# Kernel optimization log

Measured on AMD Instinct MI355X. Metric: run time of the kernel, lower is better.

Reference implementation:

```python
import jax, jax.numpy as jnp
import numpy as np

H_DIM = 256
N_HEADS = 8
HALF = H_DIM // 2

def _lin(x, W, b):
    # torch nn.Linear: y = x @ W.T + b
    y = x @ W.T
    return y + b if b is not None else y

def setup_inputs() -> dict:
    key = jax.random.key(0)
    ks = jax.random.split(key, 16)
    s = 0.02
    d = {
        'x': jax.random.normal(ks[0], (16, H_DIM, 32, 32), jnp.float32),
        'q1_w': jax.random.normal(ks[1], (HALF, HALF), jnp.float32) * s,
        'q1_b': jnp.zeros((HALF,), jnp.float32),
        'q2_w': jax.random.normal(ks[2], (HALF, HALF), jnp.float32) * s,
        'q2_b': jnp.zeros((HALF,), jnp.float32),
        'k1_w': jax.random.normal(ks[3], (HALF, HALF), jnp.float32) * s,
        'k1_b': jnp.zeros((HALF,), jnp.float32),
        'k2_w': jax.random.normal(ks[4], (HALF, HALF), jnp.float32) * s,
        'k2_b': jnp.zeros((HALF,), jnp.float32),
        'v1_w': jax.random.normal(ks[5], (HALF, HALF), jnp.float32) * s,
        'v1_b': jnp.zeros((HALF,), jnp.float32),
        'v2_w': jax.random.normal(ks[6], (HALF, HALF), jnp.float32) * s,
        'v2_b': jnp.zeros((HALF,), jnp.float32),
        'proj1_w': jax.random.normal(ks[7], (HALF, HALF), jnp.float32) * s,
        'proj1_b': jnp.zeros((HALF,), jnp.float32),
        'proj2_w': jax.random.normal(ks[8], (HALF, HALF), jnp.float32) * s,
        'proj2_b': jnp.zeros((HALF,), jnp.float32),
        'logit_scale': jnp.log(10.0 * jnp.ones((N_HEADS, 1, 1), jnp.float32)),
        'mlp_w1': jax.random.normal(ks[9], (128, 2), jnp.float32) * s,
        'mlp_b1': jnp.zeros((128,), jnp.float32),
        'mlp_w2': jax.random.normal(ks[10], (N_HEADS, 128), jnp.float32) * s,
    }
    return d

def _rel_pos_index(h, w):
    # static (numpy) relative position index, shape [N, N]
    ch, cw = np.meshgrid(np.arange(h), np.arange(w), indexing='ij')
    coords = np.stack([ch.reshape(-1), cw.reshape(-1)])  # [2, N]
    rel = coords[:, :, None] - coords[:, None, :]         # [2, N, N]
    rel = rel.transpose(1, 2, 0)
    rel[:, :, 0] += h - 1
    rel[:, :, 1] += w - 1
    return rel[:, :, 0] * (2 * w - 1) + rel[:, :, 1]

def _forward(x, q1_w, q1_b, q2_w, q2_b, k1_w, k1_b, k2_w, k2_b,
             v1_w, v1_b, v2_w, v2_b, proj1_w, proj1_b, proj2_w, proj2_b,
             logit_scale, mlp_w1, mlp_b1, mlp_w2):
    b, c, h, w = x.shape
    N = h * w
    nh = N_HEADS
    hd = c // nh
    x3 = jnp.transpose(x, (0, 2, 3, 1)).reshape(b, N, c)
    x0, x1 = x3[..., :c // 2], x3[..., c // 2:]

    def qkv(W0, b0, W1, b1):
        t = jnp.concatenate([x0 + _lin(x0, W0, b0), x1 + _lin(x1, W1, b1)], axis=-1)
        return t.reshape(b, N, nh, hd).transpose(0, 2, 1, 3)  # [b, nh, N, hd]

    q = qkv(q1_w, q1_b, q2_w, q2_b)
    k = qkv(k1_w, k1_b, k2_w, k2_b)
    v = qkv(v1_w, v1_b, v2_w, v2_b)

    eps = 1e-12
    qn = q / jnp.maximum(jnp.linalg.norm(q, axis=-1, keepdims=True), eps)
    kn = k / jnp.maximum(jnp.linalg.norm(k, axis=-1, keepdims=True), eps)
    attn = jnp.einsum('bhnd,bhmd->bhnm', qn, kn)  # cosine similarity
    scale = jnp.exp(jnp.minimum(logit_scale, jnp.log(1.0 / 0.01)))  # [nh,1,1]
    attn = attn * scale[None]

    # continuous relative-position bias (CPB) table via small MLP
    rch = jnp.arange(-(h - 1), h, dtype=jnp.float32) / (h - 1 + 1e-8)
    rcw = jnp.arange(-(w - 1), w, dtype=jnp.float32) / (w - 1 + 1e-8)
    gh, gw = jnp.meshgrid(rch, rcw, indexing='ij')
    tab = jnp.stack([gh, gw], axis=-1) * 3.2               # [2h-1, 2w-1, 2]
    tab = jnp.sign(tab) * (1.0 - jnp.exp(-jnp.abs(tab)))
    tab = jax.nn.relu(_lin(tab, mlp_w1, mlp_b1))
    tab = _lin(tab, mlp_w2, None).reshape(-1, nh)          # [(2h-1)(2w-1), nh]

    idx = jnp.asarray(_rel_pos_index(h, w))                # [N, N]
    bias = tab[idx.reshape(-1)].reshape(N, N, nh).transpose(2, 0, 1)
    bias = 16.0 * jax.nn.sigmoid(bias)
    attn = attn + bias[None]

    attn = jax.nn.softmax(attn, axis=-1)
    out = jnp.einsum('bhnm,bhmd->bhnd', attn, v).transpose(0, 2, 1, 3).reshape(b, N, c)
    o0, o1 = out[..., :c // 2], out[..., c // 2:]
    out = jnp.concatenate([_lin(o0, proj1_w, proj1_b), _lin(o1, proj2_w, proj2_b)], axis=-1)
    return out.reshape(b, h, w, c).transpose(0, 3, 1, 2)

def reference(x, q1_w, q1_b, q2_w, q2_b, k1_w, k1_b, k2_w, k2_b,
              v1_w, v1_b, v2_w, v2_b, proj1_w, proj1_b, proj2_w, proj2_b,
              logit_scale, mlp_w1, mlp_b1, mlp_w2):
    return _forward(x, q1_w, q1_b, q2_w, q2_b, k1_w, k1_b, k2_w, k2_b,
                    v1_w, v1_b, v2_w, v2_b, proj1_w, proj1_b, proj2_w, proj2_b,
                    logit_scale, mlp_w1, mlp_b1, mlp_w2)
```

## Files before the change

kernel.cpp:

```cpp
#include <hip/hip_runtime.h>
#include <cmath>


typedef _Float16 half_t;
typedef __attribute__((ext_vector_type(4))) _Float16 half4;
typedef __attribute__((ext_vector_type(8))) _Float16 half8;
typedef __attribute__((ext_vector_type(4))) float float4v;

static __device__ __forceinline__ float4v mfma16(half8 a, half8 b, float4v c) {
  return __builtin_amdgcn_mfma_f32_16x16x32_f16(a, b, c, 0, 0, 0);
}

struct PtrArr8 { const float* p[8]; };

__global__ __launch_bounds__(256) void prep_w(PtrArr8 wsrc, PtrArr8 bsrc,
                                              half_t* __restrict__ wf,
                                              float* __restrict__ bws) {
  int y = blockIdx.y;
  const float* src = nullptr;
  const float* bs = nullptr;
#pragma unroll
  for (int i = 0; i < 8; i++)
    if (i == y) { src = wsrc.p[i]; bs = bsrc.p[i]; }
  int flat = (blockIdx.x * 256 + threadIdx.x) * 4;
  float4 w = *(const float4*)(src + flat);
  int j = flat >> 7, k = flat & 127;
  if (y < 6) {
    if (k == j)     w.x += 1.0f;
    if (k + 1 == j) w.y += 1.0f;
    if (k + 2 == j) w.z += 1.0f;
    if (k + 3 == j) w.w += 1.0f;
  }
  half4 h;
  h[0] = (half_t)w.x;
  h[1] = (half_t)w.y;
  h[2] = (half_t)w.z;
  h[3] = (half_t)w.w;
  int ng = j >> 4, l = j & 15, ks = k >> 5, quad = (k >> 3) & 3, o8 = k & 7;
  *(half4*)(wf + y * 16384 + ((ng * 4 + ks) * 64 + quad * 16 + l) * 8 + o8) =
      h;
  if (blockIdx.x == 0 && threadIdx.x < 128)
    bws[y * 128 + threadIdx.x] = bs[threadIdx.x];
}

__global__ __launch_bounds__(256) void bias_mlp(const float* __restrict__ w1,
                                                const float* __restrict__ b1,
                                                const float* __restrict__ w2,
                                                const float* __restrict__ ls,
                                                float* __restrict__ tabh2) {
  __shared__ float sw1[256];
  __shared__ float sb1[128];
  __shared__ float sw2[1024];
  int t = threadIdx.x;
  sw1[t] = w1[t];
  if (t < 128) sb1[t] = b1[t];
  for (int i = t; i < 1024; i += 256) sw2[i] = w2[i];
  __syncthreads();
  int p = blockIdx.x * 256 + t;
  if (p >= 3969) return;
  int ph = p / 63, pw = p % 63;
  float t0 = (float)(ph - 31) * (3.2f / 31.0f);
  float t1 = (float)(pw - 31) * (3.2f / 31.0f);
  t0 = copysignf(1.0f - __expf(-fabsf(t0)), t0);
  t1 = copysignf(1.0f - __expf(-fabsf(t1)), t1);
  float acc[8];
#pragma unroll
  for (int hh = 0; hh < 8; hh++) acc[hh] = 0.0f;
  for (int j = 0; j < 128; j++) {
    float hj = fmaxf(0.0f, t0 * sw1[2 * j] + t1 * sw1[2 * j + 1] + sb1[j]);
#pragma unroll
    for (int hh = 0; hh < 8; hh++) acc[hh] += hj * sw2[hh * 128 + j];
  }
  const float L2E = 1.44269504f;
#pragma unroll
  for (int hh = 0; hh < 8; hh++) {
    float scale = __expf(fminf(ls[hh], 4.6051702f));
    float c14 = 14.0f - (scale + 16.0f) * L2E;
    float bias = 16.0f / (1.0f + __expf(-acc[hh]));
    tabh2[hh * 3969 + p] = bias * L2E + c14;
  }
}

__global__ __launch_bounds__(256, 4) void qkv_mfma(
    const float* __restrict__ x, const half_t* __restrict__ wfrag,
    const float* __restrict__ lscale, const float* __restrict__ bws,
    half_t* __restrict__ qf, half_t* __restrict__ kf,
    half_t* __restrict__ vf) {
  __shared__ half_t tbuf[4608];
  int t = threadIdx.x;
  int lane = t & 63, wv = t >> 6, l = lane & 15, quad = lane >> 4;
  int rw = wv & 1, cw = wv >> 1;
  int hf = blockIdx.y;
  int m0 = blockIdx.x * 32;
  int b = m0 >> 10, n0 = m0 & 1023;

  half8 afr[4];
  {
    const float* xb =
        x + ((size_t)b * 256 + hf * 128) * 1024 + n0 + rw * 16 + l;
#pragma unroll
    for (int ks = 0; ks < 4; ks++) {
      half8 a;
#pragma unroll
      for (int j = 0; j < 8; j++)
        a[j] = (half_t)xb[(size_t)(ks * 32 + quad * 8 + j) * 1024];
      afr[ks] = a;
    }
  }

  for (int op = 0; op < 3; op++) {
    int combo = op * 2 + hf;
    const half_t* wfb = wfrag + combo * 16384;
    float4v acc[4];
#pragma unroll
    for (int ngl = 0; ngl < 4; ngl++) {
      int ng = cw * 4 + ngl;
      float4v c = {0.f, 0.f, 0.f, 0.f};
#pragma unroll
      for (int ks = 0; ks < 4; ks++) {
        half8 bfrag =
            *(const half8*)(wfb + ((ng * 4 + ks) * 64 + lane) * 8);
        c = mfma16(afr[ks], bfrag, c);
      }
      acc[ngl] = c;
    }
#pragma unroll
    for (int ngl = 0; ngl < 4; ngl++) {
      float bb = bws[combo * 128 + (cw * 4 + ngl) * 16 + l];
#pragma unroll
      for (int r2 = 0; r2 < 4; r2++) acc[ngl][r2] += bb;
    }
    if (op < 2) {
#pragma unroll
      for (int hgl = 0; hgl < 2; hgl++) {
        float sc = 1.0f;
        if (op == 0)
          sc = __expf(fminf(lscale[hf * 4 + cw * 2 + hgl], 4.6051702f)) *
               1.44269504f;
#pragma unroll
        for (int r2 = 0; r2 < 4; r2++) {
          float ss = acc[2 * hgl][r2] * acc[2 * hgl][r2] +
                     acc[2 * hgl + 1][r2] * acc[2 * hgl + 1][r2];
          ss += __shfl_xor(ss, 1, 64);
          ss += __shfl_xor(ss, 2, 64);
          ss += __shfl_xor(ss, 4, 64);
          ss += __shfl_xor(ss, 8, 64);
          float rn = sc / fmaxf(sqrtf(ss), 1e-12f);
          acc[2 * hgl][r2] *= rn;
          acc[2 * hgl + 1][r2] *= rn;
        }
      }
#pragma unroll
      for (int ngl = 0; ngl < 4; ngl++)
#pragma unroll
        for (int r2 = 0; r2 < 4; r2++)
          tbuf[(rw * 16 + quad * 4 + r2) * 136 + (cw * 4 + ngl) * 16 + l] =
              (half_t)acc[ngl][r2];
      __syncthreads();
      half_t* dst = (op == 0) ? qf : kf;
#pragma unroll
      for (int i = 0; i < 2; i++) {
        int idx = t + 256 * i;
        int row = idx >> 4, colc = (idx & 15) * 8;
        half8 vv = *(const half8*)(tbuf + row * 136 + colc);
        int head = hf * 4 + (colc >> 5), d = colc & 31;
        *(half8*)(dst + (((size_t)b * 8 + head) * 1024 + n0 + row) * 32 + d) =
            vv;
      }
      __syncthreads();
    } else {
#pragma unroll
      for (int ngl = 0; ngl < 4; ngl++) {
        int col = (cw * 4 + ngl) * 16 + l;
        half4 hv;
#pragma unroll
        for (int r2 = 0; r2 < 4; r2++) hv[r2] = (half_t)acc[ngl][r2];
        *(half4*)(tbuf + col * 36 + rw * 16 + quad * 4) = hv;
      }
      __syncthreads();
#pragma unroll
      for (int i = 0; i < 8; i++) {
        int idx = t + 256 * i;
        int col = idx >> 4, rp = idx & 15;
        unsigned int val = *(const unsigned int*)(tbuf + col * 36 + rp * 2);
        int head = hf * 4 + (col >> 5);
        int d = col & 31;
        *(unsigned int*)((char*)vf +
                         (((((size_t)b * 8 + head) * 32 + d) * 1024) + n0 +
                          rp * 2) * 2) = val;
      }
    }
  }
}

__global__ __launch_bounds__(256) void attn_mfma(
    const half_t* __restrict__ qf, const half_t* __restrict__ kf,
    const half_t* __restrict__ vf, const float* __restrict__ tabh2,
    half_t* __restrict__ ao) {
  __shared__ float sb2[35 * 63];
  __shared__ half_t pa[4 * 16 * 80];

  int id = blockIdx.x;
  int qo = id >> 7;
  int bh = id & 127;
  int h = bh & 7, b = bh >> 3;
  int t = threadIdx.x;
  int lane = t & 63, wv = t >> 6, l = lane & 15, quad = lane >> 4;
  size_t bhs = (size_t)b * 8 + h;
  const half_t* kbase = kf + bhs * 1024 * 32;
  const half_t* vbase = vf + bhs * 32 * 1024;

  for (int i = t; i < 2205; i += 256)
    sb2[i] = tabh2[h * 3969 + qo * 252 + i];

  int row0 = qo * 128 + wv * 32;
  half8 qfr[2];
#pragma unroll
  for (int s = 0; s < 2; s++)
    qfr[s] = *(const half8*)(qf + (bhs * 1024 + row0 + s * 16 + l) * 32 +
                             quad * 8);

  float4v o0[2], o1[2];
  float run_l[2];
#pragma unroll
  for (int s = 0; s < 2; s++) {
    o0[s] = (float4v){0.f, 0.f, 0.f, 0.f};
    o1[s] = (float4v){0.f, 0.f, 0.f, 0.f};
    run_l[s] = 0.0f;
  }
  half_t* paw = pa + wv * 16 * 80;
  __syncthreads();

#pragma unroll 2
  for (int kt = 0; kt < 16; kt++) {
    half8 kfr[4], v0fr[2], v1fr[2];
#pragma unroll
    for (int nt = 0; nt < 4; nt++)
      kfr[nt] =
          *(const half8*)(kbase + (kt * 64 + nt * 16 + l) * 32 + quad * 8);
#pragma unroll
    for (int ks = 0; ks < 2; ks++) {
      v0fr[ks] = *(const half8*)(vbase + l * 1024 + kt * 64 + ks * 32 +
                                 quad * 8);
      v1fr[ks] = *(const half8*)(vbase + (16 + l) * 1024 + kt * 64 + ks * 32 +
                                 quad * 8);
    }
#pragma unroll
    for (int s = 0; s < 2; s++) {
      float4v sres[4];
#pragma unroll
      for (int nt = 0; nt < 4; nt++) {
        int base = (wv - 2 * kt - (nt >> 1) + 31) * 63 + s * 16 + l + 31 -
                   (nt & 1) * 16 - quad * 4;
        float4v c;
        c[0] = sb2[base];
        c[1] = sb2[base - 1];
        c[2] = sb2[base - 2];
        c[3] = sb2[base - 3];
        sres[nt] = mfma16(kfr[nt], qfr[s], c);
      }
#pragma unroll
      for (int nt = 0; nt < 4; nt++) {
        half4 ph;
#pragma unroll
        for (int r2 = 0; r2 < 4; r2++) {
          float p = exp2f(sres[nt][r2]);
          run_l[s] += p;
          ph[r2] = (half_t)p;
        }
        *(half4*)(paw + l * 80 + nt * 16 + quad * 4) = ph;
      }
#pragma unroll
      for (int ks = 0; ks < 2; ks++) {
        half8 pfr = *(const half8*)(paw + l * 80 + ks * 32 + quad * 8);
        o0[s] = mfma16(pfr, v0fr[ks], o0[s]);
        o1[s] = mfma16(pfr, v1fr[ks], o1[s]);
      }
    }
  }

#pragma unroll
  for (int s = 0; s < 2; s++) {
    float rl = run_l[s];
    rl += __shfl_xor(rl, 16, 64);
    rl += __shfl_xor(rl, 32, 64);
    float rli = 1.0f / rl;
#pragma unroll
    for (int r2 = 0; r2 < 4; r2++) {
      float linv = __shfl(rli, 20 * quad + r2, 64);
      size_t rowaddr =
          ((size_t)b * 1024 + row0 + s * 16 + quad * 4 + r2) * 256 + h * 32;
      ao[rowaddr + l] = (half_t)(o0[s][r2] * linv);
      ao[rowaddr + 16 + l] = (half_t)(o1[s][r2] * linv);
    }
  }
}

__global__ __launch_bounds__(256, 4) void proj_mfma(
    const half_t* __restrict__ ao, const half_t* __restrict__ wfrag,
    const float* __restrict__ bws, float* __restrict__ out) {
  __shared__ float yt[128 * 36];
  int t = threadIdx.x;
  int lane = t & 63, wv = t >> 6, l = lane & 15, quad = lane >> 4;
  int rw = wv & 1, cw = wv >> 1;
  int hf = blockIdx.y;
  int m0 = blockIdx.x * 32;
  int b = m0 >> 10, n0 = m0 & 1023;

  half8 afr[4];
  const half_t* ab =
      ao + ((size_t)m0 + rw * 16 + l) * 256 + hf * 128 + quad * 8;
#pragma unroll
  for (int ks = 0; ks < 4; ks++) afr[ks] = *(const half8*)(ab + ks * 32);

  const half_t* wfb = wfrag + (6 + hf) * 16384;
#pragma unroll
  for (int ngl = 0; ngl < 4; ngl++) {
    int ng = cw * 4 + ngl;
    float4v c = {0.f, 0.f, 0.f, 0.f};
#pragma unroll
    for (int ks = 0; ks < 4; ks++) {
      half8 bfrag = *(const half8*)(wfb + ((ng * 4 + ks) * 64 + lane) * 8);
      c = mfma16(afr[ks], bfrag, c);
    }
    float bb = bws[(6 + hf) * 128 + ng * 16 + l];
#pragma unroll
    for (int r2 = 0; r2 < 4; r2++) c[r2] += bb;
    *(float4v*)(yt + (ng * 16 + l) * 36 + rw * 16 + quad * 4) = c;
  }
  __syncthreads();
#pragma unroll
  for (int i = 0; i < 4; i++) {
    int idx = t + 256 * i;
    int col = idx >> 3, rg = idx & 7;
    float4v vv = *(const float4v*)(yt + col * 36 + rg * 4);
    *(float4v*)(out + ((size_t)b * 256 + hf * 128 + col) * 1024 + n0 +
                rg * 4) = vv;
  }
}

extern "C" void kernel_launch(void* const* d_in, const int* in_sizes, int n_in,
                              void* d_out, int out_size, void* d_ws,
                              size_t ws_size, hipStream_t stream) {
  (void)in_sizes; (void)n_in; (void)out_size; (void)ws_size;
  const float* x = (const float*)d_in[0];

  half_t* ws = (half_t*)d_ws;
  half_t* qfp = ws;
  half_t* kfp = ws + 4194304;
  half_t* vfp = ws + 8388608;
  half_t* aop = ws + 12582912;
  half_t* wfp = ws + 16777216;
  float* tabh2 = (float*)((char*)d_ws + 33816576);
  float* bws = (float*)((char*)d_ws + 33943584);

  PtrArr8 wsrc, bsrc;
  const int widx[8] = {1, 3, 5, 7, 9, 11, 13, 15};
  for (int i = 0; i < 8; i++) {
    wsrc.p[i] = (const float*)d_in[widx[i]];
    bsrc.p[i] = (const float*)d_in[widx[i] + 1];
  }

  prep_w<<<dim3(16, 8), 256, 0, stream>>>(wsrc, bsrc, wfp, bws);
  bias_mlp<<<16, 256, 0, stream>>>((const float*)d_in[18],
                                   (const float*)d_in[19],
                                   (const float*)d_in[20],
                                   (const float*)d_in[17], tabh2);
  qkv_mfma<<<dim3(512, 2), 256, 0, stream>>>(x, wfp, (const float*)d_in[17],
                                             bws, qfp, kfp, vfp);
  attn_mfma<<<1024, 256, 0, stream>>>(qfp, kfp, vfp, tabh2, aop);
  proj_mfma<<<dim3(512, 2), 256, 0, stream>>>(aop, wfp, bws, (float*)d_out);
}
```

Before: 186.6 us.

## Software-pipeline attention loop with KV prefetch and MFMA row-sum

Restructures the attention inner loop into a manually pipelined schedule: the next tile's K/V fragments are prefetched into double-buffered registers, and the PV product of one query sub-block is interleaved with the QK and exp of the other, using separate shared-memory P buffers per sub-block. The softmax denominator is now produced by an extra MFMA against a ones vector instead of scalar adds and shuffles. The exp results are packed with cvt_pkrtz (round-toward-zero) conversions, and launch bounds now request 4 blocks per CU. This aims to hide global-load latency and overlap MFMA with exp work, at the cost of more registers, a larger shared buffer and an extra MFMA per step.

```diff
diff --git a/kernel.cpp b/kernel.cpp
--- a/kernel.cpp
+++ b/kernel.cpp
@@ -3,9 +3,11 @@
 
 
 typedef _Float16 half_t;
+typedef __attribute__((ext_vector_type(2))) __fp16 fp16x2;
 typedef __attribute__((ext_vector_type(4))) _Float16 half4;
 typedef __attribute__((ext_vector_type(8))) _Float16 half8;
 typedef __attribute__((ext_vector_type(4))) float float4v;
+typedef __attribute__((ext_vector_type(2))) unsigned int uint2v;
 
 static __device__ __forceinline__ float4v mfma16(half8 a, half8 b, float4v c) {
   return __builtin_amdgcn_mfma_f32_16x16x32_f16(a, b, c, 0, 0, 0);
@@ -193,12 +195,79 @@
   }
 }
 
-__global__ __launch_bounds__(256) void attn_mfma(
+
+#define LOADKV(kt, VV)                                                      \
+  {                                                                         \
+    _Pragma("unroll") for (int nt = 0; nt < 4; nt++)                        \
+        kfr[nt] = *(const half8*)(kbase + ((kt)*64 + nt * 16 + l) * 32 +    \
+                                  quad * 8);                                \
+    _Pragma("unroll") for (int ks = 0; ks < 2; ks++) {                      \
+      VV[0][ks] = *(const half8*)(vbase + l * 1024 + (kt)*64 + ks * 32 +    \
+                                  quad * 8);                                \
+      VV[1][ks] = *(const half8*)(vbase + (16 + l) * 1024 + (kt)*64 +       \
+                                  ks * 32 + quad * 8);                      \
+    }                                                                       \
+  }
+
+#define QK_PHASE(kt, S, SR)                                                 \
+  {                                                                         \
+    int rowb = (wv + 31 - 2 * (kt)) * 63 + cA + (S)*16;                     \
+    _Pragma("unroll") for (int nt = 0; nt < 4; nt++) {                      \
+      int base = rowb - (nt >> 1) * 63 - (nt & 1) * 16;                     \
+      float4v c;                                                            \
+      c[0] = sb2[base];                                                     \
+      c[1] = sb2[base - 1];                                                 \
+      c[2] = sb2[base - 2];                                                 \
+      c[3] = sb2[base - 3];                                                 \
+      SR[nt] = mfma16(kfr[nt], qfr[S], c);                                  \
+    }                                                                       \
+  }
+
+#define EXP_WRITE(S, SR)                                                    \
+  {                                                                         \
+    half_t* paws = pa + (wv * 2 + (S)) * 1280;                              \
+    _Pragma("unroll") for (int nt = 0; nt < 4; nt++) {                      \
+      fp16x2 plo = __builtin_amdgcn_cvt_pkrtz(exp2f(SR[nt][0]),             \
+                                              exp2f(SR[nt][1]));            \
+      fp16x2 phi = __builtin_amdgcn_cvt_pkrtz(exp2f(SR[nt][2]),             \
+                                              exp2f(SR[nt][3]));            \
+      uint2v uu;                                                            \
+      uu.x = __builtin_bit_cast(unsigned int, plo);                         \
+      uu.y = __builtin_bit_cast(unsigned int, phi);                         \
+      *(uint2v*)(paws + l * 80 + nt * 16 + quad * 4) = uu;                  \
+    }                                                                       \
+  }
+
+#define PV_PHASE(S, VV)                                                     \
+  {                                                                         \
+    const half_t* paws = pa + (wv * 2 + (S)) * 1280;                        \
+    _Pragma("unroll") for (int ks = 0; ks < 2; ks++) {                      \
+      half8 pfr = *(const half8*)(paws + l * 80 + ks * 32 + quad * 8);      \
+      o0[S] = mfma16(pfr, VV[0][ks], o0[S]);                                \
+      o1[S] = mfma16(pfr, VV[1][ks], o1[S]);                                \
+      accl[S] = mfma16(pfr, ones, accl[S]);                                 \
+    }                                                                       \
+  }
+
+#define ITER(kt, VC, VN, DO_PREV, DO_PREF)                                  \
+  {                                                                         \
+    float4v sres[4];                                                        \
+    QK_PHASE(kt, 0, sres);                                                  \
+    if (DO_PREV) PV_PHASE(1, VN);                                           \
+    EXP_WRITE(0, sres);                                                     \
+    float4v sres2[4];                                                       \
+    QK_PHASE(kt, 1, sres2);                                                 \
+    if (DO_PREF) LOADKV((kt) + 1, VN);                                      \
+    PV_PHASE(0, VC);                                                        \
+    EXP_WRITE(1, sres2);                                                    \
+  }
+
+__global__ __launch_bounds__(256, 4) void attn_mfma(
     const half_t* __restrict__ qf, const half_t* __restrict__ kf,
     const half_t* __restrict__ vf, const float* __restrict__ tabh2,
     half_t* __restrict__ ao) {
   __shared__ float sb2[35 * 63];
-  __shared__ half_t pa[4 * 16 * 80];
+  __shared__ half_t pa[10240];
 
   int id = blockIdx.x;
   int qo = id >> 7;
@@ -209,85 +278,47 @@
   size_t bhs = (size_t)b * 8 + h;
   const half_t* kbase = kf + bhs * 1024 * 32;
   const half_t* vbase = vf + bhs * 32 * 1024;
-
-  for (int i = t; i < 2205; i += 256)
-    sb2[i] = tabh2[h * 3969 + qo * 252 + i];
-
   int row0 = qo * 128 + wv * 32;
-  half8 qfr[2];
+  int cA = l + 31 - quad * 4;
+
+  half8 kfr[4], va[2][2], vb[2][2], qfr[2];
+  LOADKV(0, va);
 #pragma unroll
   for (int s = 0; s < 2; s++)
     qfr[s] = *(const half8*)(qf + (bhs * 1024 + row0 + s * 16 + l) * 32 +
                              quad * 8);
 
-  float4v o0[2], o1[2];
-  float run_l[2];
+  for (int i = t; i < 2205; i += 256)
+    sb2[i] = tabh2[h * 3969 + qo * 252 + i];
+
+  float4v o0[2], o1[2], accl[2];
 #pragma unroll
   for (int s = 0; s < 2; s++) {
     o0[s] = (float4v){0.f, 0.f, 0.f, 0.f};
     o1[s] = (float4v){0.f, 0.f, 0.f, 0.f};
-    run_l[s] = 0.0f;
-  }
-  half_t* paw = pa + wv * 16 * 80;
+    accl[s] = (float4v){0.f, 0.f, 0.f, 0.f};
+  }
+  half8 ones;
+#pragma unroll
+  for (int j = 0; j < 8; j++) ones[j] = (half_t)1.0f;
+
   __syncthreads();
 
-#pragma unroll 2
-  for (int kt = 0; kt < 16; kt++) {
-    half8 kfr[4], v0fr[2], v1fr[2];
-#pragma unroll
-    for (int nt = 0; nt < 4; nt++)
-      kfr[nt] =
-          *(const half8*)(kbase + (kt * 64 + nt * 16 + l) * 32 + quad * 8);
-#pragma unroll
-    for (int ks = 0; ks < 2; ks++) {
-      v0fr[ks] = *(const half8*)(vbase + l * 1024 + kt * 64 + ks * 32 +
-                                 quad * 8);
-      v1fr[ks] = *(const half8*)(vbase + (16 + l) * 1024 + kt * 64 + ks * 32 +
-                                 quad * 8);
-    }
-#pragma unroll
-    for (int s = 0; s < 2; s++) {
-      float4v sres[4];
-#pragma unroll
-      for (int nt = 0; nt < 4; nt++) {
-        int base = (wv - 2 * kt - (nt >> 1) + 31) * 63 + s * 16 + l + 31 -
-                   (nt & 1) * 16 - quad * 4;
-        float4v c;
-        c[0] = sb2[base];
-        c[1] = sb2[base - 1];
-        c[2] = sb2[base - 2];
-        c[3] = sb2[base - 3];
-        sres[nt] = mfma16(kfr[nt], qfr[s], c);
-      }
-#pragma unroll
-      for (int nt = 0; nt < 4; nt++) {
-        half4 ph;
-#pragma unroll
-        for (int r2 = 0; r2 < 4; r2++) {
-          float p = exp2f(sres[nt][r2]);
-          run_l[s] += p;
-          ph[r2] = (half_t)p;
-        }
-        *(half4*)(paw + l * 80 + nt * 16 + quad * 4) = ph;
-      }
-#pragma unroll
-      for (int ks = 0; ks < 2; ks++) {
-        half8 pfr = *(const half8*)(paw + l * 80 + ks * 32 + quad * 8);
-        o0[s] = mfma16(pfr, v0fr[ks], o0[s]);
-        o1[s] = mfma16(pfr, v1fr[ks], o1[s]);
-      }
-    }
-  }
+  ITER(0, va, vb, 0, 1);
+  ITER(1, vb, va, 1, 1);
+  for (int kt2 = 2; kt2 < 14; kt2 += 2) {
+    ITER(kt2, va, vb, 1, 1);
+    ITER(kt2 + 1, vb, va, 1, 1);
+  }
+  ITER(14, va, vb, 1, 1);
+  ITER(15, vb, va, 1, 0);
+  PV_PHASE(1, vb);
 
 #pragma unroll
   for (int s = 0; s < 2; s++) {
-    float rl = run_l[s];
-    rl += __shfl_xor(rl, 16, 64);
-    rl += __shfl_xor(rl, 32, 64);
-    float rli = 1.0f / rl;
 #pragma unroll
     for (int r2 = 0; r2 < 4; r2++) {
-      float linv = __shfl(rli, 20 * quad + r2, 64);
+      float linv = 1.0f / accl[s][r2];
       size_t rowaddr =
           ((size_t)b * 1024 + row0 + s * 16 + quad * 4 + r2) * 256 + h * 32;
       ao[rowaddr + l] = (half_t)(o0[s][r2] * linv);
```

Result: slower. 205.7 us (+10.2%).
